# Performance work log

Measured on AMD Instinct MI355X. Metric: run time of the kernel, lower is better.

The kernel has to match this reference:

```python
import jax, jax.numpy as jnp
import numpy as np

L = 2
GRID_RES = 0.01
ATOL = 0.01
RTOL = 1e-5  # torch.isclose default rtol


def _grad_matrices(filtration, bar, sample_pts):
    # filtration: [S,2] simplex (x,y) filtration values
    # bar:        [P,R] bar length per sample point, per rank
    # sample_pts: [P,2] center points
    S = filtration.shape[0]
    P, R = bar.shape
    shift = jnp.arange(-L, L + 1, dtype=filtration.dtype)          # [5]
    fx = filtration[:, 0]
    fy = filtration[:, 1]
    ptx = sample_pts[:, 0]
    pty = sample_pts[:, 1]
    scale = bar + GRID_RES                                          # [P,R]
    line_x = shift[None, None, :] * scale[:, :, None] + ptx[:, None, None]  # [P,R,5]
    line_y = shift[None, None, :] * scale[:, :, None] + pty[:, None, None]  # [P,R,5]
    last_x = line_x[:, :, -1]                                       # [P,R]
    last_y = line_y[:, :, -1]                                       # [P,R]
    # torch.isclose(a, b, atol): |a-b| <= atol + rtol*|b|
    tol_x = ATOL + RTOL * jnp.abs(fx)                               # [S]
    tol_y = ATOL + RTOL * jnp.abs(fy)
    close_x = jnp.any(jnp.abs(line_x[:, :, None, :] - fx[None, None, :, None])
                      <= tol_x[None, None, :, None], axis=-1)       # [P,R,S]
    close_y = jnp.any(jnp.abs(line_y[:, :, None, :] - fy[None, None, :, None])
                      <= tol_y[None, None, :, None], axis=-1)       # [P,R,S]
    fsum = fx + fy                                                  # [S]
    psum = (ptx + pty)[:, None, None]                               # [P,1,1]
    below = fsum[None, None, :] < psum                              # [P,1,S]
    above = fsum[None, None, :] > psum
    cond_x = close_x & (fy[None, None, :] <= last_y[:, :, None])    # [P,R,S]
    cond_y = close_y & (fx[None, None, :] <= last_x[:, :, None])
    lower_x = cond_x & below
    upper_x = cond_x & above
    lower_y = cond_y & below
    upper_y = cond_y & above
    gx = jnp.where(upper_x, 1.0, jnp.where(lower_x, -1.0, 0.0))     # [P,R,S]
    gy = jnp.where(upper_y, 1.0, jnp.where(lower_y, -1.0, 0.0))
    # interleave x/y per simplex: columns (2s, 2s+1)
    gm = jnp.stack([gx, gy], axis=-1).reshape(P, R, 2 * S).transpose(1, 0, 2)  # [R,P,2S]
    any_s = lambda m: jnp.any(m, axis=2)                            # [P,R]
    cx = jnp.where(any_s(upper_x), -1.0, jnp.where(any_s(lower_x), 1.0, 0.0))
    cy = jnp.where(any_s(upper_y), -1.0, jnp.where(any_s(lower_y), 1.0, 0.0))
    gc = jnp.stack([cx, cy], axis=-1).transpose(1, 0, 2)            # [R,P,2]
    return gm, gc


def setup_inputs() -> dict:
    key = jax.random.key(0)
    k1, k2, k3, k4 = jax.random.split(key, 4)
    S, P, R = 2000, 2500, 5
    filtration = jax.random.uniform(k1, (S, 2), dtype=jnp.float32)
    bars_h0 = jax.random.uniform(k2, (P, R), dtype=jnp.float32)
    bars_h1 = jax.random.uniform(k3, (P, R), dtype=jnp.float32)
    sample_pts = jax.random.uniform(k4, (P, 2), dtype=jnp.float32)
    return {"filtration": filtration, "bars_h0": bars_h0,
            "bars_h1": bars_h1, "sample_pts": sample_pts}


def reference(filtration, bars_h0, bars_h1, sample_pts):
    # moveSimplices.forward: passes bars through and builds the sparse
    # per-point gradient matrices (the dominant compute) for H0 and H1.
    gm0, gc0 = _grad_matrices(filtration, bars_h0, sample_pts)
    gm1, gc1 = _grad_matrices(filtration, bars_h1, sample_pts)
    out = jnp.stack([bars_h0, bars_h1])  # forward returns (bars[0], bars[1])
    return out, gm0, gc0, gm1, gc1
```

## Files before the change

### kernel.cpp

```cpp
#include <hip/hip_runtime.h>

#define S 2000
#define P 2500
#define R 5

__device__ __forceinline__ void flags_for(
    float fx, float fy, float scale, float ptx, float pty,
    float lastx, float lasty, float psum,
    float& gx, float& gy, int& fl)
{
    float tolx = __fadd_rn(0.01f, __fmul_rn(1e-5f, __builtin_fabsf(fx)));
    float toly = __fadd_rn(0.01f, __fmul_rn(1e-5f, __builtin_fabsf(fy)));
    bool cx = false, cy = false;
#pragma unroll
    for (int k = -2; k <= 2; ++k) {
        float ks = (float)k * scale;
        float lx = ks + ptx;
        float ly = ks + pty;
        cx = cx || (__builtin_fabsf(lx - fx) <= tolx);
        cy = cy || (__builtin_fabsf(ly - fy) <= toly);
    }
    float fsum = fx + fy;
    bool below = fsum < psum;
    bool above = fsum > psum;
    bool condx = cx && (fy <= lasty);
    bool condy = cy && (fx <= lastx);
    bool ux = condx && above;
    bool lxf = condx && below;
    bool uy = condy && above;
    bool lyf = condy && below;
    gx = ux ? 1.0f : (lxf ? -1.0f : 0.0f);
    gy = uy ? 1.0f : (lyf ? -1.0f : 0.0f);
    fl |= (ux ? 1 : 0) | (lxf ? 2 : 0) | (uy ? 4 : 0) | (lyf ? 8 : 0);
}

__global__ __launch_bounds__(256) void grad_kernel(
    const float* __restrict__ filtration,
    const float* __restrict__ bars0,
    const float* __restrict__ bars1,
    const float* __restrict__ sample_pts,
    float* __restrict__ gm0, float* __restrict__ gc0,
    float* __restrict__ gm1, float* __restrict__ gc1)
{
    int bid = blockIdx.x;
    int h = bid / (P * R);
    int rem = bid - h * (P * R);
    int r = rem / P;
    int p = rem - r * P;

    const float* bars = h ? bars1 : bars0;
    float* gm = h ? gm1 : gm0;
    float* gc = h ? gc1 : gc0;

    float bar = bars[p * R + r];
    float scale = bar + 0.01f;
    float ptx = sample_pts[2 * p];
    float pty = sample_pts[2 * p + 1];
    float lastx = 2.0f * scale + ptx;
    float lasty = 2.0f * scale + pty;
    float psum = ptx + pty;

    float4* gmrow = (float4*)(gm + ((size_t)r * P + p) * (size_t)(2 * S));
    const float4* filt4 = (const float4*)filtration;

    __shared__ int bflags;
    if (threadIdx.x == 0) bflags = 0;
    __syncthreads();

    int myflags = 0;
    for (int j = threadIdx.x; j < S / 2; j += blockDim.x) {
        float4 f = filt4[j];
        float4 o;
        flags_for(f.x, f.y, scale, ptx, pty, lastx, lasty, psum, o.x, o.y, myflags);
        flags_for(f.z, f.w, scale, ptx, pty, lastx, lasty, psum, o.z, o.w, myflags);
        gmrow[j] = o;
    }

    int wf = 0;
    wf |= __any(myflags & 1) ? 1 : 0;
    wf |= __any(myflags & 2) ? 2 : 0;
    wf |= __any(myflags & 4) ? 4 : 0;
    wf |= __any(myflags & 8) ? 8 : 0;
    if ((threadIdx.x & 63) == 0 && wf) atomicOr(&bflags, wf);
    __syncthreads();

    if (threadIdx.x == 0) {
        int bf = bflags;
        float cxv = (bf & 1) ? -1.0f : ((bf & 2) ? 1.0f : 0.0f);
        float cyv = (bf & 4) ? -1.0f : ((bf & 8) ? 1.0f : 0.0f);
        size_t base = ((size_t)r * P + p) * 2;
        gc[base] = cxv;
        gc[base + 1] = cyv;
    }
}

__global__ __launch_bounds__(256) void copy_out_kernel(
    const float* __restrict__ b0, const float* __restrict__ b1,
    float* __restrict__ out)
{
    int i = blockIdx.x * blockDim.x + threadIdx.x;
    if (i < P * R) {
        out[i] = b0[i];
        out[P * R + i] = b1[i];
    }
}

extern "C" void kernel_launch(void* const* d_in, const int* in_sizes, int n_in,
                              void* d_out, int out_size, void* d_ws, size_t ws_size,
                              hipStream_t stream) {
    const float* filtration = (const float*)d_in[0];
    const float* bars_h0    = (const float*)d_in[1];
    const float* bars_h1    = (const float*)d_in[2];
    const float* sample_pts = (const float*)d_in[3];

    float* out = (float*)d_out;
    float* o_stack = out;
    float* gm0     = o_stack + (size_t)2 * P * R;
    float* gc0     = gm0 + (size_t)R * P * 2 * S;
    float* gm1     = gc0 + (size_t)R * P * 2;
    float* gc1     = gm1 + (size_t)R * P * 2 * S;

    copy_out_kernel<<<(P * R + 255) / 256, 256, 0, stream>>>(bars_h0, bars_h1, o_stack);
    grad_kernel<<<2 * P * R, 256, 0, stream>>>(filtration, bars_h0, bars_h1, sample_pts,
                                               gm0, gc0, gm1, gc1);
}
```

Baseline: 89.41 us.

## Process four sample points per block, reusing filtration registers with nontemporal stores

```diff
diff --git a/kernel.cpp b/kernel.cpp
--- a/kernel.cpp
+++ b/kernel.cpp
@@ -3,36 +3,12 @@
 #define S 2000
 #define P 2500
 #define R 5
+#define PT 4
+#define NPT (P / PT)
+#define HALF (S / 2)
+#define NJ 4
 
-__device__ __forceinline__ void flags_for(
-    float fx, float fy, float scale, float ptx, float pty,
-    float lastx, float lasty, float psum,
-    float& gx, float& gy, int& fl)
-{
-    float tolx = __fadd_rn(0.01f, __fmul_rn(1e-5f, __builtin_fabsf(fx)));
-    float toly = __fadd_rn(0.01f, __fmul_rn(1e-5f, __builtin_fabsf(fy)));
-    bool cx = false, cy = false;
-#pragma unroll
-    for (int k = -2; k <= 2; ++k) {
-        float ks = (float)k * scale;
-        float lx = ks + ptx;
-        float ly = ks + pty;
-        cx = cx || (__builtin_fabsf(lx - fx) <= tolx);
-        cy = cy || (__builtin_fabsf(ly - fy) <= toly);
-    }
-    float fsum = fx + fy;
-    bool below = fsum < psum;
-    bool above = fsum > psum;
-    bool condx = cx && (fy <= lasty);
-    bool condy = cy && (fx <= lastx);
-    bool ux = condx && above;
-    bool lxf = condx && below;
-    bool uy = condy && above;
-    bool lyf = condy && below;
-    gx = ux ? 1.0f : (lxf ? -1.0f : 0.0f);
-    gy = uy ? 1.0f : (lyf ? -1.0f : 0.0f);
-    fl |= (ux ? 1 : 0) | (lxf ? 2 : 0) | (uy ? 4 : 0) | (lyf ? 8 : 0);
-}
+typedef float floatx4 __attribute__((ext_vector_type(4)));
 
 __global__ __launch_bounds__(256) void grad_kernel(
     const float* __restrict__ filtration,
@@ -43,54 +19,131 @@
     float* __restrict__ gm1, float* __restrict__ gc1)
 {
     int bid = blockIdx.x;
-    int h = bid / (P * R);
-    int rem = bid - h * (P * R);
-    int r = rem / P;
-    int p = rem - r * P;
+    int h = bid / (R * NPT);
+    int rem = bid - h * (R * NPT);
+    int r = rem / NPT;
+    int pt = rem - r * NPT;
+    int p0 = pt * PT;
+    int tid = threadIdx.x;
 
     const float* bars = h ? bars1 : bars0;
     float* gm = h ? gm1 : gm0;
     float* gc = h ? gc1 : gc0;
 
-    float bar = bars[p * R + r];
-    float scale = bar + 0.01f;
-    float ptx = sample_pts[2 * p];
-    float pty = sample_pts[2 * p + 1];
-    float lastx = 2.0f * scale + ptx;
-    float lasty = 2.0f * scale + pty;
-    float psum = ptx + pty;
-
-    float4* gmrow = (float4*)(gm + ((size_t)r * P + p) * (size_t)(2 * S));
     const float4* filt4 = (const float4*)filtration;
 
-    __shared__ int bflags;
-    if (threadIdx.x == 0) bflags = 0;
+    float4 f[NJ];
+    float tx0[NJ], ty0[NJ], tx1[NJ], ty1[NJ], s0[NJ], s1[NJ];
+#pragma unroll
+    for (int it = 0; it < NJ; ++it) {
+        int j = tid + 256 * it;
+        float4 v = make_float4(0.f, 0.f, 0.f, 0.f);
+        if (j < HALF) v = filt4[j];
+        f[it] = v;
+        tx0[it] = __fadd_rn(0.01f, __fmul_rn(1e-5f, __builtin_fabsf(v.x)));
+        ty0[it] = __fadd_rn(0.01f, __fmul_rn(1e-5f, __builtin_fabsf(v.y)));
+        tx1[it] = __fadd_rn(0.01f, __fmul_rn(1e-5f, __builtin_fabsf(v.z)));
+        ty1[it] = __fadd_rn(0.01f, __fmul_rn(1e-5f, __builtin_fabsf(v.w)));
+        s0[it] = v.x + v.y;
+        s1[it] = v.z + v.w;
+    }
+
+    unsigned flags = 0;
+    size_t rowbase = ((size_t)r * P + p0) * (size_t)(2 * S);
+
+#pragma unroll
+    for (int pi = 0; pi < PT; ++pi) {
+        int p = p0 + pi;
+        float bar = bars[p * R + r];
+        float scale = bar + 0.01f;
+        float ptx = sample_pts[2 * p];
+        float pty = sample_pts[2 * p + 1];
+        float psum = ptx + pty;
+        float lxk[5], lyk[5];
+#pragma unroll
+        for (int k = 0; k < 5; ++k) {
+            float ks = (float)(k - 2) * scale;
+            lxk[k] = ks + ptx;
+            lyk[k] = ks + pty;
+        }
+        float lastx = lxk[4];
+        float lasty = lyk[4];
+
+        float axmax = 0.f, axmin = 0.f, aymax = 0.f, aymin = 0.f;
+        float* gmrow = gm + rowbase + (size_t)pi * (size_t)(2 * S);
+
+#pragma unroll
+        for (int it = 0; it < NJ; ++it) {
+            int j = tid + 256 * it;
+            if (j < HALF) {
+                floatx4 o;
+                {
+                    float fx = f[it].x, fy = f[it].y;
+                    bool cx = false, cy = false;
+#pragma unroll
+                    for (int k = 0; k < 5; ++k) {
+                        cx = cx || (__builtin_fabsf(lxk[k] - fx) <= tx0[it]);
+                        cy = cy || (__builtin_fabsf(lyk[k] - fy) <= ty0[it]);
+                    }
+                    float fsum = s0[it];
+                    bool above = fsum > psum;
+                    bool below = fsum < psum;
+                    float sgn = above ? 1.0f : (below ? -1.0f : 0.0f);
+                    bool condx = cx && (fy <= lasty);
+                    bool condy = cy && (fx <= lastx);
+                    o.x = condx ? sgn : 0.0f;
+                    o.y = condy ? sgn : 0.0f;
+                }
+                {
+                    float fx = f[it].z, fy = f[it].w;
+                    bool cx = false, cy = false;
+#pragma unroll
+                    for (int k = 0; k < 5; ++k) {
+                        cx = cx || (__builtin_fabsf(lxk[k] - fx) <= tx1[it]);
+                        cy = cy || (__builtin_fabsf(lyk[k] - fy) <= ty1[it]);
+                    }
+                    float fsum = s1[it];
+                    bool above = fsum > psum;
+                    bool below = fsum < psum;
+                    float sgn = above ? 1.0f : (below ? -1.0f : 0.0f);
+                    bool condx = cx && (fy <= lasty);
+                    bool condy = cy && (fx <= lastx);
+                    o.z = condx ? sgn : 0.0f;
+                    o.w = condy ? sgn : 0.0f;
+                }
+                axmax = fmaxf(axmax, fmaxf(o.x, o.z));
+                axmin = fminf(axmin, fminf(o.x, o.z));
+                aymax = fmaxf(aymax, fmaxf(o.y, o.w));
+                aymin = fminf(aymin, fminf(o.y, o.w));
+                __builtin_nontemporal_store(o, (floatx4*)(gmrow + (size_t)j * 4));
+            }
+        }
+        unsigned b = 0;
+        if (axmax > 0.f) b |= 1u;
+        if (axmin < 0.f) b |= 2u;
+        if (aymax > 0.f) b |= 4u;
+        if (aymin < 0.f) b |= 8u;
+        flags |= b << (4 * pi);
+    }
+
+#pragma unroll
+    for (int m = 1; m < 64; m <<= 1)
+        flags |= (unsigned)__shfl_xor((int)flags, m);
+
+    __shared__ unsigned bflags;
+    if (tid == 0) bflags = 0u;
+    __syncthreads();
+    if ((tid & 63) == 0 && flags) atomicOr(&bflags, flags);
     __syncthreads();
 
-    int myflags = 0;
-    for (int j = threadIdx.x; j < S / 2; j += blockDim.x) {
-        float4 f = filt4[j];
-        float4 o;
-        flags_for(f.x, f.y, scale, ptx, pty, lastx, lasty, psum, o.x, o.y, myflags);
-        flags_for(f.z, f.w, scale, ptx, pty, lastx, lasty, psum, o.z, o.w, myflags);
-        gmrow[j] = o;
-    }
-
-    int wf = 0;
-    wf |= __any(myflags & 1) ? 1 : 0;
-    wf |= __any(myflags & 2) ? 2 : 0;
-    wf |= __any(myflags & 4) ? 4 : 0;
-    wf |= __any(myflags & 8) ? 8 : 0;
-    if ((threadIdx.x & 63) == 0 && wf) atomicOr(&bflags, wf);
-    __syncthreads();
-
-    if (threadIdx.x == 0) {
-        int bf = bflags;
-        float cxv = (bf & 1) ? -1.0f : ((bf & 2) ? 1.0f : 0.0f);
-        float cyv = (bf & 4) ? -1.0f : ((bf & 8) ? 1.0f : 0.0f);
-        size_t base = ((size_t)r * P + p) * 2;
-        gc[base] = cxv;
-        gc[base + 1] = cyv;
+    if (tid < PT * 2) {
+        int pi = tid >> 1;
+        int c = tid & 1;
+        unsigned b = (bflags >> (4 * pi)) & 0xFu;
+        float v;
+        if (c == 0) v = (b & 1u) ? -1.0f : ((b & 2u) ? 1.0f : 0.0f);
+        else        v = (b & 4u) ? -1.0f : ((b & 8u) ? 1.0f : 0.0f);
+        gc[((size_t)r * P + p0) * 2 + tid] = v;
     }
 }
 
@@ -121,6 +174,6 @@
     float* gc1     = gm1 + (size_t)R * P * 2 * S;
 
     copy_out_kernel<<<(P * R + 255) / 256, 256, 0, stream>>>(bars_h0, bars_h1, o_stack);
-    grad_kernel<<<2 * P * R, 256, 0, stream>>>(filtration, bars_h0, bars_h1, sample_pts,
-                                               gm0, gc0, gm1, gc1);
+    grad_kernel<<<2 * R * NPT, 256, 0, stream>>>(filtration, bars_h0, bars_h1, sample_pts,
+                                                 gm0, gc0, gm1, gc1);
 }
```

Result: slower. 107.7 us (+20.5%).

## Use single-wavefront blocks, fuse bar copy, drop shared-memory flag reduction

Applied to the files above, without the earlier changes.

```diff
diff --git a/kernel.cpp b/kernel.cpp
--- a/kernel.cpp
+++ b/kernel.cpp
@@ -3,50 +3,26 @@
 #define S 2000
 #define P 2500
 #define R 5
+#define HALF (S / 2)
+#define NIT 16
 
-__device__ __forceinline__ void flags_for(
-    float fx, float fy, float scale, float ptx, float pty,
-    float lastx, float lasty, float psum,
-    float& gx, float& gy, int& fl)
-{
-    float tolx = __fadd_rn(0.01f, __fmul_rn(1e-5f, __builtin_fabsf(fx)));
-    float toly = __fadd_rn(0.01f, __fmul_rn(1e-5f, __builtin_fabsf(fy)));
-    bool cx = false, cy = false;
-#pragma unroll
-    for (int k = -2; k <= 2; ++k) {
-        float ks = (float)k * scale;
-        float lx = ks + ptx;
-        float ly = ks + pty;
-        cx = cx || (__builtin_fabsf(lx - fx) <= tolx);
-        cy = cy || (__builtin_fabsf(ly - fy) <= toly);
-    }
-    float fsum = fx + fy;
-    bool below = fsum < psum;
-    bool above = fsum > psum;
-    bool condx = cx && (fy <= lasty);
-    bool condy = cy && (fx <= lastx);
-    bool ux = condx && above;
-    bool lxf = condx && below;
-    bool uy = condy && above;
-    bool lyf = condy && below;
-    gx = ux ? 1.0f : (lxf ? -1.0f : 0.0f);
-    gy = uy ? 1.0f : (lyf ? -1.0f : 0.0f);
-    fl |= (ux ? 1 : 0) | (lxf ? 2 : 0) | (uy ? 4 : 0) | (lyf ? 8 : 0);
-}
+typedef float floatx4 __attribute__((ext_vector_type(4)));
 
-__global__ __launch_bounds__(256) void grad_kernel(
+__global__ __launch_bounds__(64) void grad_kernel(
     const float* __restrict__ filtration,
     const float* __restrict__ bars0,
     const float* __restrict__ bars1,
     const float* __restrict__ sample_pts,
+    float* __restrict__ out,
     float* __restrict__ gm0, float* __restrict__ gc0,
     float* __restrict__ gm1, float* __restrict__ gc1)
 {
     int bid = blockIdx.x;
-    int h = bid / (P * R);
-    int rem = bid - h * (P * R);
+    int h = bid / (R * P);
+    int rem = bid - h * (R * P);
     int r = rem / P;
     int p = rem - r * P;
+    int lane = threadIdx.x;
 
     const float* bars = h ? bars1 : bars0;
     float* gm = h ? gm1 : gm0;
@@ -56,52 +32,82 @@
     float scale = bar + 0.01f;
     float ptx = sample_pts[2 * p];
     float pty = sample_pts[2 * p + 1];
-    float lastx = 2.0f * scale + ptx;
-    float lasty = 2.0f * scale + pty;
     float psum = ptx + pty;
 
-    float4* gmrow = (float4*)(gm + ((size_t)r * P + p) * (size_t)(2 * S));
-    const float4* filt4 = (const float4*)filtration;
+    float lxk[5], lyk[5];
+#pragma unroll
+    for (int k = 0; k < 5; ++k) {
+        float ks = (float)(k - 2) * scale;
+        lxk[k] = ks + ptx;
+        lyk[k] = ks + pty;
+    }
+    float lastx = lxk[4];
+    float lasty = lyk[4];
 
-    __shared__ int bflags;
-    if (threadIdx.x == 0) bflags = 0;
-    __syncthreads();
+    if (lane == 0) out[(size_t)h * P * R + p * R + r] = bar;
 
-    int myflags = 0;
-    for (int j = threadIdx.x; j < S / 2; j += blockDim.x) {
-        float4 f = filt4[j];
-        float4 o;
-        flags_for(f.x, f.y, scale, ptx, pty, lastx, lasty, psum, o.x, o.y, myflags);
-        flags_for(f.z, f.w, scale, ptx, pty, lastx, lasty, psum, o.z, o.w, myflags);
-        gmrow[j] = o;
+    const floatx4* filt4 = (const floatx4*)filtration;
+    float* gmrow = gm + ((size_t)r * P + p) * (size_t)(2 * S);
+
+    float axmax = 0.f, axmin = 0.f, aymax = 0.f, aymin = 0.f;
+
+#pragma unroll
+    for (int it = 0; it < NIT; ++it) {
+        int j = lane + 64 * it;
+        if (it < NIT - 1 || j < HALF) {
+            floatx4 f = filt4[j];
+            floatx4 o;
+            {
+                float fx = f.x, fy = f.y;
+                float tolx = __fadd_rn(0.01f, __fmul_rn(1e-5f, __builtin_fabsf(fx)));
+                float toly = __fadd_rn(0.01f, __fmul_rn(1e-5f, __builtin_fabsf(fy)));
+                bool cx = false, cy = false;
+#pragma unroll
+                for (int k = 0; k < 5; ++k) {
+                    cx = cx || (__builtin_fabsf(lxk[k] - fx) <= tolx);
+                    cy = cy || (__builtin_fabsf(lyk[k] - fy) <= toly);
+                }
+                float fsum = fx + fy;
+                bool above = fsum > psum;
+                bool below = fsum < psum;
+                float sgn = above ? 1.0f : (below ? -1.0f : 0.0f);
+                o.x = (cx && (fy <= lasty)) ? sgn : 0.0f;
+                o.y = (cy && (fx <= lastx)) ? sgn : 0.0f;
+            }
+            {
+                float fx = f.z, fy = f.w;
+                float tolx = __fadd_rn(0.01f, __fmul_rn(1e-5f, __builtin_fabsf(fx)));
+                float toly = __fadd_rn(0.01f, __fmul_rn(1e-5f, __builtin_fabsf(fy)));
+                bool cx = false, cy = false;
+#pragma unroll
+                for (int k = 0; k < 5; ++k) {
+                    cx = cx || (__builtin_fabsf(lxk[k] - fx) <= tolx);
+                    cy = cy || (__builtin_fabsf(lyk[k] - fy) <= toly);
+                }
+                float fsum = fx + fy;
+                bool above = fsum > psum;
+                bool below = fsum < psum;
+                float sgn = above ? 1.0f : (below ? -1.0f : 0.0f);
+                o.z = (cx && (fy <= lasty)) ? sgn : 0.0f;
+                o.w = (cy && (fx <= lastx)) ? sgn : 0.0f;
+            }
+            axmax = fmaxf(axmax, fmaxf(o.x, o.z));
+            axmin = fminf(axmin, fminf(o.x, o.z));
+            aymax = fmaxf(aymax, fmaxf(o.y, o.w));
+            aymin = fminf(aymin, fminf(o.y, o.w));
+            *(floatx4*)(gmrow + (size_t)j * 4) = o;
+        }
     }
 
-    int wf = 0;
-    wf |= __any(myflags & 1) ? 1 : 0;
-    wf |= __any(myflags & 2) ? 2 : 0;
-    wf |= __any(myflags & 4) ? 4 : 0;
-    wf |= __any(myflags & 8) ? 8 : 0;
-    if ((threadIdx.x & 63) == 0 && wf) atomicOr(&bflags, wf);
-    __syncthreads();
-
-    if (threadIdx.x == 0) {
-        int bf = bflags;
-        float cxv = (bf & 1) ? -1.0f : ((bf & 2) ? 1.0f : 0.0f);
-        float cyv = (bf & 4) ? -1.0f : ((bf & 8) ? 1.0f : 0.0f);
-        size_t base = ((size_t)r * P + p) * 2;
-        gc[base] = cxv;
-        gc[base + 1] = cyv;
-    }
-}
-
-__global__ __launch_bounds__(256) void copy_out_kernel(
-    const float* __restrict__ b0, const float* __restrict__ b1,
-    float* __restrict__ out)
-{
-    int i = blockIdx.x * blockDim.x + threadIdx.x;
-    if (i < P * R) {
-        out[i] = b0[i];
-        out[P * R + i] = b1[i];
+    bool anyUx = __any(axmax > 0.f);
+    bool anyLx = __any(axmin < 0.f);
+    bool anyUy = __any(aymax > 0.f);
+    bool anyLy = __any(aymin < 0.f);
+    if (lane == 0) {
+        float cxv = anyUx ? -1.0f : (anyLx ? 1.0f : 0.0f);
+        float cyv = anyUy ? -1.0f : (anyLy ? 1.0f : 0.0f);
+        float2 v = make_float2(cxv, cyv);
+        *(float2*)(gc + ((size_t)r * P + p) * 2) = v;
     }
 }
 
@@ -120,7 +126,6 @@
     float* gm1     = gc0 + (size_t)R * P * 2;
     float* gc1     = gm1 + (size_t)R * P * 2 * S;
 
-    copy_out_kernel<<<(P * R + 255) / 256, 256, 0, stream>>>(bars_h0, bars_h1, o_stack);
-    grad_kernel<<<2 * P * R, 256, 0, stream>>>(filtration, bars_h0, bars_h1, sample_pts,
-                                               gm0, gc0, gm1, gc1);
+    grad_kernel<<<2 * R * P, 64, 0, stream>>>(filtration, bars_h0, bars_h1, sample_pts,
+                                              o_stack, gm0, gc0, gm1, gc1);
 }
```

After: 88.48 us. Within noise of the previous version (-1.0%).
